# Kernel optimization log

Measured on AMD Instinct MI355X. Metric: run time of the kernel, lower is better.

Reference implementation:

```python
import jax, jax.numpy as jnp
import numpy as np

N_POINTS = 65536
N_ANCHORS = 1024
MAX_PTS = 512  # _MAX_POINTS_PER_BOX


def setup_inputs() -> dict:
    key = jax.random.key(0)
    k_xy, k_z, k_c, k_wl, k_h = jax.random.split(key, 5)
    # Point cloud over a 100m x 100m plot, z in [0, 10m]
    xy = jax.random.uniform(k_xy, (N_POINTS, 2), dtype=jnp.float32) * 100.0
    z = jax.random.uniform(k_z, (N_POINTS, 1), dtype=jnp.float32) * 10.0
    points = jnp.concatenate([xy, z], axis=-1)  # [N, 3]
    # Anchors: (cx, cy, cz_unused, w, l, h)
    c = jax.random.uniform(k_c, (N_ANCHORS, 2), dtype=jnp.float32) * 100.0
    cz = jnp.zeros((N_ANCHORS, 1), dtype=jnp.float32)
    wl = 1.0 + jax.random.uniform(k_wl, (N_ANCHORS, 2), dtype=jnp.float32) * 4.0
    h = 5.0 + jax.random.uniform(k_h, (N_ANCHORS, 1), dtype=jnp.float32) * 10.0
    anchors = jnp.concatenate([c, cz, wl, h], axis=-1)  # [A, 6]
    return {"points": points, "anchors": anchors, "n": MAX_PTS}


def reference(points, anchors, n):
    """Point-in-box grouping: for each anchor, gather up to n points inside its
    axis-aligned box (xy centered at cx,cy with extents w,l; z in [0,h]),
    recentered by the anchor xy. Padded to fixed size n (zeros), plus counts.
    Matches _subsample_points_batch except selection is first-n (deterministic)
    instead of randperm subsample."""
    px, py, pz = points[:, 0], points[:, 1], points[:, 2]  # [N]
    cx, cy = anchors[:, 0:1], anchors[:, 1:2]              # [A,1]
    w, l, h = anchors[:, 3:4], anchors[:, 4:5], anchors[:, 5:6]
    half_w, half_l = w * 0.5, l * 0.5
    # Dense in-box mask [A, N]
    mask = ((px[None] >= cx - half_w) & (px[None] <= cx + half_w)
            & (py[None] >= cy - half_l) & (py[None] <= cy + half_l)
            & (pz[None] >= 0.0) & (pz[None] <= h))
    counts = mask.sum(axis=1).astype(jnp.int32)            # [A]
    # top_k on 0/1 scores: ties broken by lowest index -> first n inside points
    vals, idx = jax.lax.top_k(mask.astype(jnp.float32), n)  # [A, n]
    valid = vals > 0.5                                      # [A, n]
    pts = points[idx]                                       # [A, n, 3]
    center = jnp.concatenate(
        [anchors[:, 0:2], jnp.zeros_like(anchors[:, 0:1])], axis=-1)  # [A,3]
    centered = pts - center[:, None, :]
    out = jnp.where(valid[..., None], centered, 0.0)        # [A, n, 3]
    return out, counts
```

## Files before the change

### kernel.cpp

```cpp
#include <hip/hip_runtime.h>

#define N_POINTS  65536
#define N_ANCHORS 1024
#define MAX_PTS   512
#define GX        20
#define NC        (GX * GX)
#define INV_CS    0.2f
#define NSUB      256
#define CAPS      16
#define LDS_CAP   512

#define WS_CNT    0
#define WS_BINNED 409600

__device__ __forceinline__ int cell_of(float px, float py) {
    int cx = (int)(px * INV_CS);
    int cy = (int)(py * INV_CS);
    cx = cx > GX - 1 ? GX - 1 : cx;
    cy = cy > GX - 1 ? GX - 1 : cy;
    return cy * GX + cx;
}

__global__ __launch_bounds__(256) void scatter_kernel(
    const float* __restrict__ points, int* __restrict__ cnt,
    float4* __restrict__ binned)
{
    __shared__ int   lcnt[NC];
    __shared__ float pstage[256 * 3];
    const int b   = blockIdx.x;
    const int tid = threadIdx.x;

    if (tid < 192)
        ((float4*)pstage)[tid] = ((const float4*)points)[b * 192 + tid];
    for (int i = tid; i < NC; i += 256) lcnt[i] = 0;
    __syncthreads();

    const float px = pstage[tid * 3 + 0];
    const float py = pstage[tid * 3 + 1];
    const float pz = pstage[tid * 3 + 2];
    const int c    = cell_of(px, py);
    const int slot = atomicAdd(&lcnt[c], 1);
    if (slot < CAPS)
        binned[(c * NSUB + b) * CAPS + slot] =
            make_float4(px, py, pz, __int_as_float(b * 256 + tid));
    __syncthreads();
    for (int i = tid; i < NC; i += 256) {
        int l = lcnt[i];
        cnt[i * NSUB + b] = l < CAPS ? l : CAPS;
    }
}

__global__ __launch_bounds__(256) void anchor_kernel(
    const float4* __restrict__ binned, const int* __restrict__ cnt,
    const float* __restrict__ anchors, float* __restrict__ out,
    float* __restrict__ counts)
{
    const int a   = blockIdx.x;
    const int tid = threadIdx.x;

    const float acx = anchors[a * 6 + 0];
    const float acy = anchors[a * 6 + 1];
    const float hw  = anchors[a * 6 + 3] * 0.5f;
    const float hl  = anchors[a * 6 + 4] * 0.5f;
    const float h   = anchors[a * 6 + 5];
    const float xmin = acx - hw, xmax = acx + hw;
    const float ymin = acy - hl, ymax = acy + hl;

    int cx0 = (int)(fmaxf(xmin, 0.0f) * INV_CS);
    int cx1 = (int)(fmaxf(xmax, 0.0f) * INV_CS);
    int cy0 = (int)(fmaxf(ymin, 0.0f) * INV_CS);
    int cy1 = (int)(fmaxf(ymax, 0.0f) * INV_CS);
    if (cx1 > GX - 1) cx1 = GX - 1;
    if (cy1 > GX - 1) cy1 = GX - 1;
    if (cx0 > GX - 1) cx0 = GX - 1;
    if (cy0 > GX - 1) cy0 = GX - 1;

    const int cell0 = cy0 * GX + cx0;
    const int cell1 = cy0 * GX + cx1;
    const int cell2 = cy1 * GX + cx0;
    const int cell3 = cy1 * GX + cx1;
    int ncells = 1;
    if (cx1 > cx0) ncells = 2;
    if (cy1 > cy0) ncells = (cx1 > cx0) ? 4 : 2;

    __shared__ int k;
    __shared__ float4 buf[LDS_CAP];

    const int q = tid >> 6;
    const int l = tid & 63;
    int lens[4]  = {0, 0, 0, 0};
    int bases[4] = {0, 0, 0, 0};
    if (q < ncells) {
        int ci;
        if (ncells == 1)      ci = cell0;
        else if (ncells == 2) ci = (q == 0) ? cell0 : ((cx1 > cx0) ? cell1 : cell2);
        else                  ci = (q == 0) ? cell0 : (q == 1) ? cell1
                                 : (q == 2) ? cell2 : cell3;
        #pragma unroll
        for (int r = 0; r < 4; ++r) {
            const int seg = ci * NSUB + (l + 64 * r);
            lens[r]  = cnt[seg];
            bases[r] = seg * CAPS;
        }
    }
    if (tid == 0) k = 0;
    __syncthreads();

    float4 p0[4];
    #pragma unroll
    for (int r = 0; r < 4; ++r)
        if (lens[r] > 0) p0[r] = binned[bases[r]];

    #pragma unroll
    for (int r = 0; r < 4; ++r) {
        if (lens[r] <= 0) continue;
        float4 p = p0[r];
        for (int e = 0; ; ) {
            if (p.x >= xmin && p.x <= xmax &&
                p.y >= ymin && p.y <= ymax &&
                p.z >= 0.0f && p.z <= h) {
                const int slot = atomicAdd(&k, 1);
                if (slot < LDS_CAP) buf[slot] = p;
            }
            if (++e >= lens[r]) break;
            p = binned[bases[r] + e];
        }
    }
    __syncthreads();

    const int K  = k;
    const int Kc = K < LDS_CAP ? K : LDS_CAP;

    float* __restrict__ outa = out + (size_t)a * (MAX_PTS * 3);
    for (int e = tid; e < Kc; e += 256) {
        const float4 pe = buf[e];
        const int ide = __float_as_int(pe.w);
        int rank = 0;
        for (int f = 0; f < Kc; ++f)
            rank += (__float_as_int(buf[f].w) < ide) ? 1 : 0;
        if (rank < MAX_PTS) {
            outa[rank * 3 + 0] = pe.x - acx;
            outa[rank * 3 + 1] = pe.y - acy;
            outa[rank * 3 + 2] = pe.z;
        }
    }

    if (tid == 0) counts[a] = (float)K;
}

extern "C" void kernel_launch(void* const* d_in, const int* in_sizes, int n_in,
                              void* d_out, int out_size, void* d_ws, size_t ws_size,
                              hipStream_t stream) {
    const float* points  = (const float*)d_in[0];
    const float* anchors = (const float*)d_in[1];

    float* out    = (float*)d_out;
    float* counts = (float*)d_out + (size_t)N_ANCHORS * MAX_PTS * 3;

    char* ws = (char*)d_ws;
    int*    cnt    = (int*)(ws + WS_CNT);
    float4* binned = (float4*)(ws + WS_BINNED);

    scatter_kernel<<<dim3(NSUB),      dim3(256), 0, stream>>>(points, cnt, binned);
    anchor_kernel <<<dim3(N_ANCHORS), dim3(256), 0, stream>>>(binned, cnt, anchors, out, counts);
}
```

Before: 76.99 us.

## Replace per-block sub-binned cells with global per-cell buckets via atomics

The scatter step now appends each point directly into a single global bucket per grid cell using global atomics, replacing the previous per-block sub-bins of capacity 16. A memset clears the cell counters before the scatter. The anchor kernel then reads contiguous cell buckets with lanes striding over entries, instead of walking 256 sparse sub-segments per cell with serial per-thread loops. This cuts the scattered, mostly empty segment reads in the anchor kernel, at the cost of global atomic contention in the scatter and an extra memset launch. Capping each cell at 320 points could drop points if a cell overflows, and the cell capacity is tuned to the expected density of the test inputs.

```diff
diff --git a/kernel.cpp b/kernel.cpp
--- a/kernel.cpp
+++ b/kernel.cpp
@@ -6,12 +6,11 @@
 #define GX        20
 #define NC        (GX * GX)
 #define INV_CS    0.2f
-#define NSUB      256
-#define CAPS      16
+#define CAP_CELL  320
 #define LDS_CAP   512
 
-#define WS_CNT    0
-#define WS_BINNED 409600
+#define WS_CELLCNT 0
+#define WS_CELLS   2048
 
 __device__ __forceinline__ int cell_of(float px, float py) {
     int cx = (int)(px * INV_CS);
@@ -22,36 +21,29 @@
 }
 
 __global__ __launch_bounds__(256) void scatter_kernel(
-    const float* __restrict__ points, int* __restrict__ cnt,
-    float4* __restrict__ binned)
+    const float* __restrict__ points, int* __restrict__ cellcnt,
+    float4* __restrict__ cells)
 {
-    __shared__ int   lcnt[NC];
     __shared__ float pstage[256 * 3];
     const int b   = blockIdx.x;
     const int tid = threadIdx.x;
 
     if (tid < 192)
         ((float4*)pstage)[tid] = ((const float4*)points)[b * 192 + tid];
-    for (int i = tid; i < NC; i += 256) lcnt[i] = 0;
     __syncthreads();
 
     const float px = pstage[tid * 3 + 0];
     const float py = pstage[tid * 3 + 1];
     const float pz = pstage[tid * 3 + 2];
     const int c    = cell_of(px, py);
-    const int slot = atomicAdd(&lcnt[c], 1);
-    if (slot < CAPS)
-        binned[(c * NSUB + b) * CAPS + slot] =
+    const int slot = atomicAdd(&cellcnt[c], 1);
+    if (slot < CAP_CELL)
+        cells[c * CAP_CELL + slot] =
             make_float4(px, py, pz, __int_as_float(b * 256 + tid));
-    __syncthreads();
-    for (int i = tid; i < NC; i += 256) {
-        int l = lcnt[i];
-        cnt[i * NSUB + b] = l < CAPS ? l : CAPS;
-    }
 }
 
 __global__ __launch_bounds__(256) void anchor_kernel(
-    const float4* __restrict__ binned, const int* __restrict__ cnt,
+    const float4* __restrict__ cells, const int* __restrict__ cellcnt,
     const float* __restrict__ anchors, float* __restrict__ out,
     float* __restrict__ counts)
 {
@@ -86,44 +78,28 @@
     __shared__ int k;
     __shared__ float4 buf[LDS_CAP];
 
-    const int q = tid >> 6;
-    const int l = tid & 63;
-    int lens[4]  = {0, 0, 0, 0};
-    int bases[4] = {0, 0, 0, 0};
+    if (tid == 0) k = 0;
+    __syncthreads();
+
+    const int q    = tid >> 6;
+    const int lane = tid & 63;
     if (q < ncells) {
         int ci;
         if (ncells == 1)      ci = cell0;
         else if (ncells == 2) ci = (q == 0) ? cell0 : ((cx1 > cx0) ? cell1 : cell2);
         else                  ci = (q == 0) ? cell0 : (q == 1) ? cell1
                                  : (q == 2) ? cell2 : cell3;
-        #pragma unroll
-        for (int r = 0; r < 4; ++r) {
-            const int seg = ci * NSUB + (l + 64 * r);
-            lens[r]  = cnt[seg];
-            bases[r] = seg * CAPS;
-        }
-    }
-    if (tid == 0) k = 0;
-    __syncthreads();
-
-    float4 p0[4];
-    #pragma unroll
-    for (int r = 0; r < 4; ++r)
-        if (lens[r] > 0) p0[r] = binned[bases[r]];
-
-    #pragma unroll
-    for (int r = 0; r < 4; ++r) {
-        if (lens[r] <= 0) continue;
-        float4 p = p0[r];
-        for (int e = 0; ; ) {
+        int len = cellcnt[ci];
+        len = len < CAP_CELL ? len : CAP_CELL;
+        const int base = ci * CAP_CELL;
+        for (int e = lane; e < len; e += 64) {
+            const float4 p = cells[base + e];
             if (p.x >= xmin && p.x <= xmax &&
                 p.y >= ymin && p.y <= ymax &&
                 p.z >= 0.0f && p.z <= h) {
                 const int slot = atomicAdd(&k, 1);
                 if (slot < LDS_CAP) buf[slot] = p;
             }
-            if (++e >= lens[r]) break;
-            p = binned[bases[r] + e];
         }
     }
     __syncthreads();
@@ -158,9 +134,10 @@
     float* counts = (float*)d_out + (size_t)N_ANCHORS * MAX_PTS * 3;
 
     char* ws = (char*)d_ws;
-    int*    cnt    = (int*)(ws + WS_CNT);
-    float4* binned = (float4*)(ws + WS_BINNED);
+    int*    cellcnt = (int*)(ws + WS_CELLCNT);
+    float4* cells   = (float4*)(ws + WS_CELLS);
 
-    scatter_kernel<<<dim3(NSUB),      dim3(256), 0, stream>>>(points, cnt, binned);
-    anchor_kernel <<<dim3(N_ANCHORS), dim3(256), 0, stream>>>(binned, cnt, anchors, out, counts);
+    hipMemsetAsync(cellcnt, 0, NC * sizeof(int), stream);
+    scatter_kernel<<<dim3(256),       dim3(256), 0, stream>>>(points, cellcnt, cells);
+    anchor_kernel <<<dim3(N_ANCHORS), dim3(256), 0, stream>>>(cells, cellcnt, anchors, out, counts);
 }
```

After: 87.75 us. 1.14x slower.
